# Kernel optimization log

Measured on AMD Instinct MI355X. Metric: run time of the kernel, lower is better.

Reference implementation:

```python
import jax, jax.numpy as jnp
import numpy as np

EPS = 1e-5

def layer_norm(x, g, b):
    m = jnp.mean(x, axis=-1, keepdims=True)
    v = jnp.mean((x - m) ** 2, axis=-1, keepdims=True)
    return (x - m) * jax.lax.rsqrt(v + EPS) * g + b

def conv1d(x, w, b, pad):
    # x: [B, C_in, L], w: [C_out, C_in, K]
    y = jax.lax.conv_general_dilated(x, w, (1,), [(pad, pad)],
                                     dimension_numbers=('NCH', 'OIH', 'NCH'))
    return y + b[None, :, None]

def setup_inputs() -> dict:
    key = jax.random.key(0)
    B, L, D, H, W, HID = 8, 1024, 512, 8, 3, 64
    ks = jax.random.split(key, 32)
    s = 0.02
    inp = {}
    inp['x'] = jax.random.normal(ks[0], (B, L, D), jnp.float32)
    # WaveDetector convs
    inp['conv1_w'] = jax.random.normal(ks[1], (HID, D, 5), jnp.float32) * s
    inp['conv1_b'] = jnp.zeros((HID,), jnp.float32)
    inp['conv2_w'] = jax.random.normal(ks[2], (HID, HID, 3), jnp.float32) * s
    inp['conv2_b'] = jnp.zeros((HID,), jnp.float32)
    inp['conv3_w'] = jax.random.normal(ks[3], (W, HID, 3), jnp.float32) * s
    inp['conv3_b'] = jnp.zeros((W,), jnp.float32)
    # wave type embedding
    inp['wave_emb'] = jax.random.normal(ks[4], (W, D), jnp.float32) * s
    # attention projections (stored as [in, out])
    inp['wq_w'] = jax.random.normal(ks[5], (D, D), jnp.float32) * s
    inp['wq_b'] = jnp.zeros((D,), jnp.float32)
    inp['wk_w'] = jax.random.normal(ks[6], (D, D), jnp.float32) * s
    inp['wk_b'] = jnp.zeros((D,), jnp.float32)
    inp['wv_w'] = jax.random.normal(ks[7], (D, D), jnp.float32) * s
    inp['wv_b'] = jnp.zeros((D,), jnp.float32)
    # gate MLP: D -> D//4 -> H
    inp['g1_w'] = jax.random.normal(ks[8], (D, D // 4), jnp.float32) * s
    inp['g1_b'] = jnp.zeros((D // 4,), jnp.float32)
    inp['g2_w'] = jax.random.normal(ks[9], (D // 4, H), jnp.float32) * s
    inp['g2_b'] = jnp.zeros((H,), jnp.float32)
    # layer norms
    for i, nm in enumerate(['ln_attn', 'norm1', 'ln_conv', 'norm2', 'norm3']):
        inp[nm + '_g'] = jnp.ones((D,), jnp.float32) + jax.random.normal(ks[10 + i], (D,), jnp.float32) * 0.01
        inp[nm + '_b'] = jax.random.normal(ks[15 + i], (D,), jnp.float32) * 0.01
    # subgraph conv: one Linear per wave + wave weights
    inp['wc_w'] = jax.random.normal(ks[20], (W, D, D), jnp.float32) * s
    inp['wc_b'] = jnp.zeros((W, D), jnp.float32)
    inp['wave_weights'] = jnp.ones((W,), jnp.float32) / W
    # FFN
    inp['f1_w'] = jax.random.normal(ks[21], (D, 4 * D), jnp.float32) * s
    inp['f1_b'] = jnp.zeros((4 * D,), jnp.float32)
    inp['f2_w'] = jax.random.normal(ks[22], (4 * D, D), jnp.float32) * s
    inp['f2_b'] = jnp.zeros((D,), jnp.float32)
    return inp

def reference(x, conv1_w, conv1_b, conv2_w, conv2_b, conv3_w, conv3_b, wave_emb,
              wq_w, wq_b, wk_w, wk_b, wv_w, wv_b, g1_w, g1_b, g2_w, g2_b,
              ln_attn_g, ln_attn_b, norm1_g, norm1_b, wc_w, wc_b, wave_weights,
              ln_conv_g, ln_conv_b, norm2_g, norm2_b, f1_w, f1_b, f2_w, f2_b,
              norm3_g, norm3_b):
    B, L, D = x.shape
    H = g2_w.shape[1]
    hd = D // H
    # --- WaveDetector ---
    xt = jnp.swapaxes(x, 1, 2)                       # [B, D, L]
    h = jax.nn.relu(conv1d(xt, conv1_w, conv1_b, 2))
    h = jax.nn.relu(conv1d(h, conv2_w, conv2_b, 1))
    wp = conv1d(h, conv3_w, conv3_b, 1)              # [B, W, L]
    wave_mask = jax.nn.softmax(jnp.swapaxes(wp, 1, 2), axis=-1)  # [B, L, W]
    # --- WaveTypeEncoding ---
    labels = jnp.argmax(wave_mask, axis=-1)          # [B, L] int
    x = x + wave_emb[labels]
    # --- subgraph adjacency (base_adj = ones) ---
    wave_sim = jnp.einsum('blw,bmw->blm', wave_mask, wave_mask)  # [B, L, L]
    subgraph_adj = wave_sim
    # --- DynamicWaveAttention ---
    residual = x
    Q = (x @ wq_w + wq_b).reshape(B, L, H, hd)
    K = (x @ wk_w + wk_b).reshape(B, L, H, hd)
    V = (x @ wv_w + wv_b).reshape(B, L, H, hd)
    scores = jnp.einsum('bqhd,bkhd->bhqk', Q, K) / (hd ** 0.5)
    gates = jax.nn.sigmoid(jax.nn.relu(x @ g1_w + g1_b) @ g2_w + g2_b)  # [B, L, H]
    gates = jnp.transpose(gates, (0, 2, 1))[:, :, None, :]              # [B, H, 1, L]
    scores = scores * gates + scores * wave_sim[:, None]
    scores = scores + subgraph_adj[:, None]
    attn = jax.nn.softmax(scores, axis=-1)
    attn_out = jnp.einsum('bhqk,bkhd->bqhd', attn, V).reshape(B, L, D)
    attn_out = layer_norm(attn_out + residual, ln_attn_g, ln_attn_b)
    x = layer_norm(x + attn_out, norm1_g, norm1_b)
    # --- ECGSubGraphConv (adj_matrices=None path) ---
    feats = jnp.einsum('bld,wdo->blwo', x, wc_w) + wc_b          # [B, L, W, D]
    conv_out = jnp.einsum('blwo,blw,w->blo', feats, wave_mask, wave_weights)
    conv_out = layer_norm(jax.nn.relu(conv_out), ln_conv_g, ln_conv_b)
    x = layer_norm(x + conv_out, norm2_g, norm2_b)
    # --- FFN ---
    ffn = jax.nn.relu(x @ f1_w + f1_b) @ f2_w + f2_b
    x = layer_norm(x + ffn, norm3_g, norm3_b)
    return (x, wave_mask, subgraph_adj)
```

## Files before the change

kernel.cpp:

```cpp
#include <hip/hip_runtime.h>

typedef unsigned short u16;
typedef unsigned int u32;
typedef __attribute__((ext_vector_type(8))) short bf16x8;
typedef __attribute__((ext_vector_type(4))) float f32x4;
typedef __attribute__((ext_vector_type(4))) u32 u32x4;

#define DEVI static __device__ __forceinline__

constexpr size_t OFF_WTQKV = 0;
constexpr size_t OFF_G1T   = 1572864;
constexpr size_t OFF_G2T   = OFF_G1T + 131072;
constexpr size_t OFF_WCT   = OFF_G2T + 2048;
constexpr size_t OFF_F1T   = OFF_WCT + 1572864;
constexpr size_t OFF_F2T   = OFF_F1T + 2097152;
constexpr size_t OFF_W1R   = OFF_F2T + 2097152;
constexpr size_t OFF_W2R   = OFF_W1R + 655360;
constexpr size_t OFF_H1    = OFF_W2R + 49152;
constexpr size_t OFF_GMID  = OFF_H1;
constexpr size_t OFF_GATES = OFF_H1 + 2097152;
constexpr size_t OFF_X1    = OFF_GATES + 262144;
constexpr size_t OFF_X3    = OFF_X1;
constexpr size_t OFF_X1B   = OFF_X1 + 16777216;
constexpr size_t OFF_FMID  = OFF_X1B;
constexpr size_t OFF_Q     = OFF_X1B + 8388608;
constexpr size_t OFF_H1P   = OFF_Q;
constexpr size_t OFF_K     = OFF_Q + 8388608;
constexpr size_t OFF_XH    = OFF_K;
constexpr size_t OFF_VT    = OFF_K + 8388608;
constexpr size_t OFF_XL    = OFF_VT + 32768;
constexpr size_t OFF_AO    = OFF_VT + 8388608;
constexpr size_t OFF_CONV  = OFF_AO;
constexpr size_t OFF_FP0   = OFF_AO;
constexpr size_t OFF_X2    = OFF_AO + 16777216;
constexpr size_t OFF_FP1   = OFF_X2;
constexpr size_t OFF_X2B   = OFF_X2 + 16777216;
constexpr size_t OFF_X3B   = OFF_X2B;

DEVI u16 f2bf(float f) {
  u32 u = __builtin_bit_cast(u32, f);
  u32 r = (u + 0x7FFFu + ((u >> 16) & 1u)) >> 16;
  return (u16)r;
}
DEVI float bf2f(u16 h) { u32 u = ((u32)h) << 16; return __builtin_bit_cast(float, u); }

DEVI void load8(const float* __restrict__ p, float o[8]) {
  const float4* q = (const float4*)p;
  float4 a = q[0], b = q[1];
  o[0]=a.x; o[1]=a.y; o[2]=a.z; o[3]=a.w; o[4]=b.x; o[5]=b.y; o[6]=b.z; o[7]=b.w;
}
DEVI void store8(float* __restrict__ p, const float o[8]) {
  float4 a; a.x=o[0]; a.y=o[1]; a.z=o[2]; a.w=o[3];
  float4 b; b.x=o[4]; b.y=o[5]; b.z=o[6]; b.w=o[7];
  float4* q = (float4*)p; q[0]=a; q[1]=b;
}
DEVI void store8bf(u16* __restrict__ p, const float o[8]) {
  u32 w[4];
#pragma unroll
  for (int i=0;i<4;i++) w[i] = (u32)f2bf(o[2*i]) | ((u32)f2bf(o[2*i+1]) << 16);
  u32x4 v; v.x=w[0]; v.y=w[1]; v.z=w[2]; v.w=w[3];
  *(u32x4*)p = v;
}

DEVI void gl_lds16(const u16* g, u16* l) {
  __builtin_amdgcn_global_load_lds((const __attribute__((address_space(1))) u32*)g,
                                   (__attribute__((address_space(3))) u32*)l, 16, 0, 0);
}

#define PIPE_WAIT(N)  asm volatile("s_waitcnt vmcnt(%0)" :: "n"(N) : "memory")
#define PIPE_WAIT0()  asm volatile("s_waitcnt vmcnt(0)" ::: "memory")
#define PIPE_BAR()    do { __builtin_amdgcn_s_barrier(); asm volatile("" ::: "memory"); } while (0)
#define PIPE_BAR_LGKM() do { asm volatile("s_waitcnt lgkmcnt(0)" ::: "memory"); \
                             __builtin_amdgcn_s_barrier(); asm volatile("" ::: "memory"); } while (0)

__global__ __launch_bounds__(64) void prep_kernel(
    const float* s0, const float* s1, const float* s2, const float* s3, const float* s4,
    const float* s5, const float* s6, const float* s7, const float* s8, const float* s9,
    char* ws) {
  const int jsrc[11] = {0,1,2,3,4, 5,5,5, 6,7, 9};
  const int jK[11]   = {512,512,512,512,128, 512,512,512, 512,2048, 64};
  const int jN[11]   = {512,512,512,128,8,   512,512,512, 2048,512, 192};
  const int jSo[11]  = {0,0,0,0,0, 0,262144,524288, 0,0, 0};
  const long long jDo[11] = {
    (long long)OFF_WTQKV, (long long)(OFF_WTQKV+524288), (long long)(OFF_WTQKV+1048576),
    (long long)OFF_G1T, (long long)OFF_G2T,
    (long long)OFF_WCT, (long long)(OFF_WCT+524288), (long long)(OFF_WCT+1048576),
    (long long)OFF_F1T, (long long)OFF_F2T, (long long)OFF_W2R};
  const int jF[11]   = {0,0,0,0,0,0,0,0,0,0,1};

  int blk = blockIdx.x;
  int j = 0, t = 0;
  for (int i = 0; i < 11; i++) {
    int cnt = ((jK[i] + 63) >> 6) * ((jN[i] + 63) >> 6);
    if (blk < cnt) { j = i; t = blk; break; }
    blk -= cnt;
  }
  int K = jK[j], N = jN[j];
  int ktiles = (K + 63) >> 6;
  int k0 = (t % ktiles) << 6, n0 = (t / ktiles) << 6;
  const float* SS[10] = {s0,s1,s2,s3,s4,s5,s6,s7,s8,s9};
  const float* src = SS[jsrc[j]] + jSo[j];
  __shared__ float tile[64][65];
  int tt = threadIdx.x;
  for (int i = 0; i < 64; i++) {
    float v = 0.f;
    if (k0 + i < K && n0 + tt < N) v = src[(size_t)(k0 + i) * N + n0 + tt];
    tile[i][tt] = v;
  }
  __syncthreads();
  if (jF[j]) {
    float* dst = (float*)(ws + jDo[j]);
    for (int i = 0; i < 64; i++)
      if (n0 + i < N && k0 + tt < K) dst[(size_t)(n0 + i) * K + k0 + tt] = tile[tt][i];
  } else {
    u16* dst = (u16*)(ws + jDo[j]);
    for (int i = 0; i < 64; i++)
      if (n0 + i < N && k0 + tt < K) dst[(size_t)(n0 + i) * K + k0 + tt] = f2bf(tile[tt][i]);
  }
}

__global__ __launch_bounds__(256) void wprep_kernel(const float* __restrict__ w1,
                                                    u16* __restrict__ wh, u16* __restrict__ wl) {
  int c = blockIdx.x;
  for (int kk = threadIdx.x; kk < 2560; kk += 256) {
    int k = kk >> 9, d = kk & 511;
    float v = w1[(size_t)c * 2560 + d * 5 + k];
    u16 h = f2bf(v);
    wh[(size_t)c * 2560 + kk] = h;
    wl[(size_t)c * 2560 + kk] = f2bf(v - bf2f(h));
  }
}

__global__ __launch_bounds__(256) void xsplit_kernel(const float* __restrict__ x,
                                                     u16* __restrict__ xh, u16* __restrict__ xl) {
  int idx = blockIdx.x * 256 + threadIdx.x;
  if (idx >= 8 * 1028 * 64) return;
  int r = idx >> 6;
  int col = (idx & 63) * 8;
  int b = r / 1028, rr = r % 1028;
  size_t dof = ((size_t)r) * 512 + col;
  if (rr < 2 || rr >= 1026) {
    u32x4 z; z.x = 0; z.y = 0; z.z = 0; z.w = 0;
    *(u32x4*)&xh[dof] = z;
    *(u32x4*)&xl[dof] = z;
    return;
  }
  const float* src = x + (((size_t)b << 10) + rr - 2) * 512 + col;
  float v[8];
  load8(src, v);
  u32 wh_[4], wl_[4];
#pragma unroll
  for (int i = 0; i < 4; i++) {
    u16 h0 = f2bf(v[2 * i]),     l0 = f2bf(v[2 * i]     - bf2f(f2bf(v[2 * i])));
    u16 h1 = f2bf(v[2 * i + 1]), l1 = f2bf(v[2 * i + 1] - bf2f(f2bf(v[2 * i + 1])));
    wh_[i] = (u32)h0 | ((u32)h1 << 16);
    wl_[i] = (u32)l0 | ((u32)l1 << 16);
  }
  u32x4 H; H.x=wh_[0]; H.y=wh_[1]; H.z=wh_[2]; H.w=wh_[3];
  u32x4 L; L.x=wl_[0]; L.y=wl_[1]; L.z=wl_[2]; L.w=wl_[3];
  *(u32x4*)&xh[dof] = H;
  *(u32x4*)&xl[dof] = L;
}

__global__ __launch_bounds__(256, 6) void conv1g_kernel(
    const u16* __restrict__ xh, const u16* __restrict__ xl,
    const u16* __restrict__ wh, const u16* __restrict__ wl,
    float* __restrict__ h1p) {
  __shared__ alignas(16) u16 a_s[2][64 * 32];
  __shared__ alignas(16) u16 b_s[2][64 * 32];
  const int tid = threadIdx.x, lane = tid & 63, wid = tid >> 6;
  const int m0 = blockIdx.x * 64;
  const int z = blockIdx.z;
  const int wr = wid >> 1, wc = wid & 1;
  const int mb = wr * 32, nb = wc * 32;
  const int lrow = lane & 15, lk = (lane >> 4) * 8;
  const int lr4 = lane >> 2, lc8 = (lane & 3) * 8;
  const int bb = m0 >> 10, lblk = m0 & 1023;
  const size_t xrow0 = (size_t)bb * 1028;

  auto stage = [&](int buf, int kk) {
    int p = (kk >= 5120) ? 2 : (kk >= 2560) ? 1 : 0;
    int kpp = kk - p * 2560;
    int ktap = kpp >> 9, d0 = kpp & 511;
    const u16* xa = (p == 1) ? xl : xh;
    const u16* wb = (p == 2) ? wl : wh;
    gl_lds16(&xa[(xrow0 + lblk + wid * 16 + lr4 + ktap) * 512 + d0 + lc8],
             &a_s[buf][wid * 512]);
    gl_lds16(&wb[(size_t)(wid * 16 + lr4) * 2560 + kpp + lc8],
             &b_s[buf][wid * 512]);
  };

  f32x4 acc[2][2];
#pragma unroll
  for (int m = 0; m < 2; m++)
#pragma unroll
    for (int n = 0; n < 2; n++) { acc[m][n].x=0.f; acc[m][n].y=0.f; acc[m][n].z=0.f; acc[m][n].w=0.f; }

  const int kz0 = z * 1920, kz1 = kz0 + 1920;
  stage(0, kz0);
  int cur = 0;
  for (int kk = kz0; kk < kz1; kk += 32) {
    if (kk + 32 < kz1) {
      stage(cur ^ 1, kk + 32);
      PIPE_WAIT(2);
    } else {
      PIPE_WAIT0();
    }
    PIPE_BAR();
    bf16x8 af[2], bfr[2];
#pragma unroll
    for (int m = 0; m < 2; m++) af[m]  = *(const bf16x8*)&a_s[cur][(mb + m * 16 + lrow) * 32 + lk];
#pragma unroll
    for (int n = 0; n < 2; n++) bfr[n] = *(const bf16x8*)&b_s[cur][(nb + n * 16 + lrow) * 32 + lk];
#pragma unroll
    for (int m = 0; m < 2; m++)
#pragma unroll
      for (int n = 0; n < 2; n++)
        acc[m][n] = __builtin_amdgcn_mfma_f32_16x16x32_bf16(af[m], bfr[n], acc[m][n], 0, 0, 0);
    PIPE_BAR_LGKM();
    cur ^= 1;
  }
  const int r4 = (lane >> 4) * 4;
#pragma unroll
  for (int m = 0; m < 2; m++) {
#pragma unroll
    for (int n = 0; n < 2; n++) {
      const int col = nb + n * 16 + lrow;
#pragma unroll
      for (int j = 0; j < 4; j++) {
        const int row = m0 + mb + m * 16 + r4 + j;
        h1p[(size_t)z * 524288 + (size_t)row * 64 + col] = acc[m][n][j];
      }
    }
  }
}

__global__ __launch_bounds__(256) void conv23_kernel(
    const float* __restrict__ h1p, const float* __restrict__ b1,
    const float* __restrict__ w2r, const float* __restrict__ b2,
    const float* __restrict__ w3, const float* __restrict__ b3,
    const float* __restrict__ x, const float* __restrict__ emb,
    float* __restrict__ wmOut, float* __restrict__ x1, u16* __restrict__ x1b) {
  int seg = blockIdx.x;
  int batch = seg >> 5, l0 = (seg & 31) << 5;
  int tid = threadIdx.x, lane = tid & 63, wave = tid >> 6;
  __shared__ float hs[36][64];
  __shared__ float h2s[34][65];
  __shared__ float w3s[576];
  __shared__ int labS[32];
  for (int i = tid; i < 36 * 64; i += 256) {
    int r = i >> 6, cc = i & 63;
    int lp = l0 - 2 + r;
    float v = 0.f;
    if (lp >= 0 && lp < 1024) {
      size_t base = ((size_t)batch * 1024 + lp) * 64 + cc;
      float s = b1[cc];
#pragma unroll
      for (int q = 0; q < 4; q++) s += h1p[base + (size_t)q * 524288];
      v = fmaxf(s, 0.f);
    }
    hs[r][cc] = v;
  }
  for (int i = tid; i < 576; i += 256) w3s[i] = w3[i];
  __syncthreads();
  {
    int c = lane;
    int r0 = wave * 9;
    float a2[9];
#pragma unroll
    for (int i = 0; i < 9; i++) a2[i] = b2[c];
    for (int dd = 0; dd < 64; dd++) {
      float xv[11];
#pragma unroll
      for (int i = 0; i < 11; i++) xv[i] = (r0 + i < 36) ? hs[r0 + i][dd] : 0.f;
#pragma unroll
      for (int k = 0; k < 3; k++) {
        float wv = w2r[(size_t)(dd * 3 + k) * 64 + c];
#pragma unroll
        for (int i = 0; i < 9; i++) a2[i] += xv[i + k] * wv;
      }
    }
#pragma unroll
    for (int i = 0; i < 9; i++) {
      int hr = r0 + i;
      if (hr < 34) h2s[hr][c] = fmaxf(a2[i], 0.f);
    }
  }
  __syncthreads();
  if (tid < 32) {
    float wp[3];
#pragma unroll
    for (int jw = 0; jw < 3; jw++) {
      float a = b3[jw];
      for (int k = 0; k < 3; k++)
        for (int cc = 0; cc < 64; cc++)
          a += h2s[tid + k][cc] * w3s[(jw * 64 + cc) * 3 + k];
      wp[jw] = a;
    }
    float mx = fmaxf(wp[0], fmaxf(wp[1], wp[2]));
    float e0 = __expf(wp[0] - mx), e1 = __expf(wp[1] - mx), e2 = __expf(wp[2] - mx);
    float inv = 1.f / (e0 + e1 + e2);
    size_t mo = ((size_t)batch * 1024 + l0 + tid) * 3;
    wmOut[mo] = e0 * inv; wmOut[mo + 1] = e1 * inv; wmOut[mo + 2] = e2 * inv;
    int lb = 0; float bv = wp[0];
    if (wp[1] > bv) { bv = wp[1]; lb = 1; }
    if (wp[2] > bv) { lb = 2; }
    labS[tid] = lb;
  }
  __syncthreads();
  for (int i = tid; i < 32 * 512; i += 256) {
    int r = i >> 9, cc = i & 511;
    size_t gi = ((size_t)batch * 1024 + l0 + r) * 512 + cc;
    float v = x[gi] + emb[labS[r] * 512 + cc];
    x1[gi] = v;
    x1b[gi] = f2bf(v);
  }
}

__global__ __launch_bounds__(256) void wavesim_kernel(const float* __restrict__ wm,
                                                      float* __restrict__ adj) {
  int b = blockIdx.x >> 7;
  int r0 = (blockIdx.x & 127) << 3;
  __shared__ float ms[1024][3];
  int tid = threadIdx.x;
  for (int i = tid; i < 3072; i += 256) ms[i / 3][i % 3] = wm[(size_t)b * 3072 + i];
  __syncthreads();
  for (int r = 0; r < 8; r++) {
    float a0 = ms[r0 + r][0], a1 = ms[r0 + r][1], a2 = ms[r0 + r][2];
    for (int m = tid; m < 1024; m += 256)
      adj[((size_t)b * 1024 + r0 + r) * 1024 + m] = a0 * ms[m][0] + a1 * ms[m][1] + a2 * ms[m][2];
  }
}

struct GemmArgs {
  const u16* A; const u16* Bt;
  int lda; int ldb; int K;
  const float* bias;
  u16* obf; int ldo;
  float* of32; int ldo32;
  u16* Qo; u16* Ko; u16* Vto;
  const float* bq; const float* bk; const float* bv;
};

template<int BM, int BN, int FM, int FN, int EPI>
__global__ __launch_bounds__(256, 3) void gemm_k(GemmArgs p) {
  __shared__ alignas(16) u16 a_s[2][BM * 32];
  __shared__ alignas(16) u16 b_s[2][BN * 32];
  const int tid = threadIdx.x;
  const int lane = tid & 63, wid = tid >> 6;
  const int m0 = blockIdx.x * BM, n0 = blockIdx.y * BN;
  const int koff = (EPI == 6) ? blockIdx.z * p.K : 0;
  const int wr = wid >> 1, wc = wid & 1;
  const int mb = wr * (FM * 16), nb = wc * (FN * 16);
  const int lrow = lane & 15, lk = (lane >> 4) * 8;
  constexpr int CPW_A = BM / 64;
  constexpr int CPW_B = BN / 64;
  constexpr int NL = CPW_A + CPW_B;
  const int lr4 = lane >> 2, lc8 = (lane & 3) * 8;

  auto stage = [&](int buf, int k0) {
#pragma unroll
    for (int j = 0; j < CPW_A; j++) {
      int chunk = wid * CPW_A + j;
      gl_lds16(&p.A[(size_t)(m0 + chunk * 16 + lr4) * p.lda + koff + k0 + lc8],
               &a_s[buf][chunk * 512]);
    }
#pragma unroll
    for (int j = 0; j < CPW_B; j++) {
      int chunk = wid * CPW_B + j;
      gl_lds16(&p.Bt[(size_t)(n0 + chunk * 16 + lr4) * p.ldb + koff + k0 + lc8],
               &b_s[buf][chunk * 512]);
    }
  };

  f32x4 acc[FM][FN];
#pragma unroll
  for (int m = 0; m < FM; m++)
#pragma unroll
    for (int n = 0; n < FN; n++) { acc[m][n].x=0.f; acc[m][n].y=0.f; acc[m][n].z=0.f; acc[m][n].w=0.f; }

  stage(0, 0);
  int cur = 0;
  for (int k0 = 0; k0 < p.K; k0 += 32) {
    if (k0 + 32 < p.K) {
      stage(cur ^ 1, k0 + 32);
      PIPE_WAIT(NL);
    } else {
      PIPE_WAIT0();
    }
    PIPE_BAR();
    bf16x8 af[FM], bfr[FN];
#pragma unroll
    for (int m = 0; m < FM; m++) af[m] = *(const bf16x8*)&a_s[cur][(mb + m * 16 + lrow) * 32 + lk];
#pragma unroll
    for (int n = 0; n < FN; n++) bfr[n] = *(const bf16x8*)&b_s[cur][(nb + n * 16 + lrow) * 32 + lk];
#pragma unroll
    for (int m = 0; m < FM; m++)
#pragma unroll
      for (int n = 0; n < FN; n++)
        acc[m][n] = __builtin_amdgcn_mfma_f32_16x16x32_bf16(af[m], bfr[n], acc[m][n], 0, 0, 0);
    PIPE_BAR_LGKM();
    cur ^= 1;
  }
  const int r4 = (lane >> 4) * 4;
#pragma unroll
  for (int m = 0; m < FM; m++) {
#pragma unroll
    for (int n = 0; n < FN; n++) {
      const int col = n0 + nb + n * 16 + lrow;
#pragma unroll
      for (int j = 0; j < 4; j++) {
        const int row = m0 + mb + m * 16 + r4 + j;
        float v = acc[m][n][j];
        if constexpr (EPI == 1) {
          v += p.bias[col];
          v = fmaxf(v, 0.f);
          p.obf[(size_t)row * p.ldo + col] = f2bf(v);
        } else if constexpr (EPI == 2) {
          v += p.bias[col];
          p.of32[(size_t)row * p.ldo32 + col] = v;
        } else if constexpr (EPI == 3) {
          if (col < 512) {
            v += p.bq[col];
            p.Qo[(size_t)row * 512 + col] = f2bf(v);
          } else if (col < 1024) {
            int cc = col - 512;
            v += p.bk[cc];
            p.Ko[(size_t)row * 512 + cc] = f2bf(v);
          } else if (col < 1536) {
            int cc = col - 1024;
            v += p.bv[cc];
            int hh = cc >> 6, dd = cc & 63;
            int bb2 = row >> 10, ll = row & 1023;
            p.Vto[((((size_t)bb2 * 8 + hh) * 64 + dd) << 10) + ll] = f2bf(v);
          } else {
            int cc = col - 1536;
            v += p.bias[cc];
            v = fmaxf(v, 0.f);
            p.obf[(size_t)row * 128 + cc] = f2bf(v);
          }
        } else if constexpr (EPI == 6) {
          if (blockIdx.z == 0) v += p.bias[col];
          p.of32[(size_t)blockIdx.z * p.ldo32 + (size_t)row * 512 + col] = v;
        }
      }
    }
  }
}

__global__ __launch_bounds__(256) void wcg_kernel(
    const u16* __restrict__ A, const u16* __restrict__ Wct,
    const float* __restrict__ wcb, const float* __restrict__ wmask,
    const float* __restrict__ wwts, float* __restrict__ out) {
  __shared__ alignas(16) u16 a_s[2][128 * 32];
  __shared__ alignas(16) u16 b_s[2][3 * 64 * 32];
  const int tid = threadIdx.x, lane = tid & 63, wid = tid >> 6;
  const int m0 = blockIdx.x * 128, n0 = blockIdx.y * 64;
  const int wr = wid >> 1, wc = wid & 1;
  const int mb = wr * 64, nb = wc * 32;
  const int lrow = lane & 15, lk = (lane >> 4) * 8;
  const int lr4 = lane >> 2, lc8 = (lane & 3) * 8;

  auto stage = [&](int buf, int k0) {
#pragma unroll
    for (int t = 0; t < 2; t++) {
      int ch = wid * 2 + t;
      gl_lds16(&A[(size_t)(m0 + ch * 16 + lr4) * 512 + k0 + lc8], &a_s[buf][ch * 512]);
    }
#pragma unroll
    for (int t = 0; t < 3; t++) {
      int ch = wid * 3 + t;
      int wI = ch >> 2, sub = ch & 3;
      gl_lds16(&Wct[(size_t)wI * 262144 + (size_t)(n0 + sub * 16 + lr4) * 512 + k0 + lc8],
               &b_s[buf][ch * 512]);
    }
  };

  f32x4 acc[4][2][3];
#pragma unroll
  for (int m = 0; m < 4; m++)
#pragma unroll
    for (int n = 0; n < 2; n++)
#pragma unroll
      for (int w = 0; w < 3; w++) { acc[m][n][w].x=0.f; acc[m][n][w].y=0.f; acc[m][n][w].z=0.f; acc[m][n][w].w=0.f; }

  stage(0, 0);
  int cur = 0;
  for (int k0 = 0; k0 < 512; k0 += 32) {
    if (k0 + 32 < 512) {
      stage(cur ^ 1, k0 + 32);
      PIPE_WAIT(5);
    } else {
      PIPE_WAIT0();
    }
    PIPE_BAR();
    bf16x8 af[4], bfr[3][2];
#pragma unroll
    for (int m = 0; m < 4; m++) af[m] = *(const bf16x8*)&a_s[cur][(mb + m * 16 + lrow) * 32 + lk];
#pragma unroll
    for (int w = 0; w < 3; w++)
#pragma unroll
      for (int n = 0; n < 2; n++)
        bfr[w][n] = *(const bf16x8*)&b_s[cur][(w * 64 + nb + n * 16 + lrow) * 32 + lk];
#pragma unroll
    for (int m = 0; m < 4; m++)
#pragma unroll
      for (int n = 0; n < 2; n++)
#pragma unroll
        for (int w = 0; w < 3; w++)
          acc[m][n][w] = __builtin_amdgcn_mfma_f32_16x16x32_bf16(af[m], bfr[w][n], acc[m][n][w], 0, 0, 0);
    PIPE_BAR_LGKM();
    cur ^= 1;
  }
  const float w0 = wwts[0], w1 = wwts[1], w2 = wwts[2];
  const int r4 = (lane >> 4) * 4;
#pragma unroll
  for (int m = 0; m < 4; m++) {
#pragma unroll
    for (int j = 0; j < 4; j++) {
      const int row = m0 + mb + m * 16 + r4 + j;
      float c0 = wmask[(size_t)row * 3 + 0] * w0;
      float c1 = wmask[(size_t)row * 3 + 1] * w1;
      float c2 = wmask[(size_t)row * 3 + 2] * w2;
#pragma unroll
      for (int n = 0; n < 2; n++) {
        const int col = n0 + nb + n * 16 + lrow;
        float v = c0 * (acc[m][n][0][j] + wcb[col])
                + c1 * (acc[m][n][1][j] + wcb[512 + col])
                + c2 * (acc[m][n][2][j] + wcb[1024 + col]);
        out[(size_t)row * 512 + col] = v;
      }
    }
  }
}

__global__ __launch_bounds__(256) void gates2_kernel(const u16* __restrict__ gmid,
    const u16* __restrict__ g2t, const float* __restrict__ g2b, float* __restrict__ gates) {
  int r0 = blockIdx.x * 64;
  __shared__ u16 ms[64][136];
  __shared__ u16 gs[8][136];
  __shared__ float gb[8];
  int tid = threadIdx.x;
  for (int i = tid; i < 1024; i += 256) {
    int r = i >> 4, ch = (i & 15) * 8;
    *(bf16x8*)&ms[r][ch] = *(const bf16x8*)&gmid[(size_t)(r0 + r) * 128 + ch];
  }
  if (tid < 128) {
    int r = tid >> 4, ch = (tid & 15) * 8;
    *(bf16x8*)&gs[r][ch] = *(const bf16x8*)&g2t[(size_t)r * 128 + ch];
  }
  if (tid < 8) gb[tid] = g2b[tid];
  __syncthreads();
  for (int o = tid; o < 512; o += 256) {
    int r = o >> 3, hh = o & 7;
    float a = gb[hh];
    for (int k = 0; k < 128; k++) a += bf2f(ms[r][k]) * bf2f(gs[hh][k]);
    gates[(size_t)(r0 + r) * 8 + hh] = 1.f / (1.f + __expf(-a));
  }
}

__global__ __launch_bounds__(256, 4) void attn_kernel(
    const u16* __restrict__ Qb, const u16* __restrict__ Kb, const u16* __restrict__ Vt,
    const float* __restrict__ gates, const float* __restrict__ wm, float* __restrict__ ao) {
  const int g = blockIdx.x & 63, qt = blockIdx.x >> 6;
  const int b = g >> 3, h = g & 7, q0 = qt << 6;
  const int tid = threadIdx.x, lane = tid & 63, w = tid >> 6;
  __shared__ alignas(16) u16 k_s[64 * 64];
  __shared__ alignas(16) u16 v_s[64 * 64];
  __shared__ u16 p_s[4][16][72];
  __shared__ float gat[64];
  __shared__ float wmk[64][4];
  const int lrow = lane & 15, lq = lane >> 4, lk = lq * 8;
  const int qrb = q0 + w * 16;
  const int sr_ = lane >> 3, sc_ = lane & 7;
  bf16x8 qf[2];
#pragma unroll
  for (int ks = 0; ks < 2; ks++)
    qf[ks] = *(const bf16x8*)&Qb[((size_t)(b * 1024 + qrb + lrow)) * 512 + h * 64 + ks * 32 + lk];
  float wq_[4][3];
#pragma unroll
  for (int j = 0; j < 4; j++) {
    int qr = qrb + lq * 4 + j;
#pragma unroll
    for (int t = 0; t < 3; t++) wq_[j][t] = wm[((size_t)b * 1024 + qr) * 3 + t];
  }
  float lsum[4];
  f32x4 oacc[4];
#pragma unroll
  for (int j = 0; j < 4; j++) lsum[j] = 0.f;
#pragma unroll
  for (int n = 0; n < 4; n++) { oacc[n].x=0.f; oacc[n].y=0.f; oacc[n].z=0.f; oacc[n].w=0.f; }

  const u16* Kbase = Kb + ((size_t)b * 1024) * 512 + h * 64;
  const u16* Vbase = Vt + ((size_t)(b * 8 + h)) * 64 * 1024;

  for (int kt = 0; kt < 16; kt++) {
    int k0 = kt * 64;
    __syncthreads();
#pragma unroll
    for (int t = 0; t < 2; t++) {
      int ch = (w << 1) | t;
      int r = (ch << 3) | sr_;
      int srcc = ((sc_ ^ (r & 7)) << 3);
      gl_lds16(&Kbase[(size_t)(k0 + r) * 512 + srcc], &k_s[ch << 9]);
      gl_lds16(&Vbase[(size_t)r * 1024 + k0 + srcc], &v_s[ch << 9]);
    }
    if (tid < 64) {
      gat[tid] = gates[((size_t)b * 1024 + k0 + tid) * 8 + h];
#pragma unroll
      for (int t = 0; t < 3; t++) wmk[tid][t] = wm[((size_t)b * 1024 + k0 + tid) * 3 + t];
    }
    __syncthreads();
    f32x4 s[4];
#pragma unroll
    for (int n = 0; n < 4; n++) { s[n].x=0.f; s[n].y=0.f; s[n].z=0.f; s[n].w=0.f; }
#pragma unroll
    for (int ks = 0; ks < 2; ks++) {
      bf16x8 kf[4];
#pragma unroll
      for (int n = 0; n < 4; n++) {
        int kr = n * 16 + lrow;
        kf[n] = *(const bf16x8*)&k_s[kr * 64 + ((((ks << 2) | lq) ^ (kr & 7)) << 3)];
      }
#pragma unroll
      for (int n = 0; n < 4; n++)
        s[n] = __builtin_amdgcn_mfma_f32_16x16x32_bf16(qf[ks], kf[n], s[n], 0, 0, 0);
    }
    float pv[4][4];
#pragma unroll
    for (int n = 0; n < 4; n++) {
      int cl = n * 16 + lrow;
      float gg = gat[cl];
      float w0 = wmk[cl][0], w1 = wmk[cl][1], w2 = wmk[cl][2];
#pragma unroll
      for (int j = 0; j < 4; j++) {
        float wsv = wq_[j][0] * w0 + wq_[j][1] * w1 + wq_[j][2] * w2;
        float sv = s[n][j] * 0.125f;
        float e = __expf(sv * (gg + wsv) + wsv);
        pv[n][j] = e;
        lsum[j] += e;
      }
    }
#pragma unroll
    for (int n = 0; n < 4; n++)
#pragma unroll
      for (int j = 0; j < 4; j++)
        p_s[w][lq * 4 + j][n * 16 + lrow] = f2bf(pv[n][j]);
#pragma unroll
    for (int ks = 0; ks < 2; ks++) {
      bf16x8 pa, vb[4];
      pa = *(const bf16x8*)&p_s[w][lrow][ks * 32 + lk];
#pragma unroll
      for (int n = 0; n < 4; n++) {
        int vr = n * 16 + lrow;
        vb[n] = *(const bf16x8*)&v_s[vr * 64 + ((((ks << 2) | lq) ^ (vr & 7)) << 3)];
      }
#pragma unroll
      for (int n = 0; n < 4; n++)
        oacc[n] = __builtin_amdgcn_mfma_f32_16x16x32_bf16(pa, vb[n], oacc[n], 0, 0, 0);
    }
  }
  float rinv[4];
#pragma unroll
  for (int j = 0; j < 4; j++) {
    float s = lsum[j];
#pragma unroll
    for (int d = 1; d < 16; d <<= 1) s += __shfl_xor(s, d);
    rinv[j] = 1.f / s;
  }
#pragma unroll
  for (int n = 0; n < 4; n++) {
    int col = h * 64 + n * 16 + lrow;
#pragma unroll
    for (int j = 0; j < 4; j++) {
      int row = b * 1024 + qrb + lq * 4 + j;
      ao[(size_t)row * 512 + col] = oacc[n][j] * rinv[j];
    }
  }
}

DEVI void ln512(const float u[8], const float* __restrict__ g, const float* __restrict__ b,
                int lane, float out[8]) {
  float s = 0.f;
#pragma unroll
  for (int i = 0; i < 8; i++) s += u[i];
#pragma unroll
  for (int m = 1; m < 64; m <<= 1) s += __shfl_xor(s, m);
  float mean = s * (1.f / 512.f);
  float d[8], q = 0.f;
#pragma unroll
  for (int i = 0; i < 8; i++) { d[i] = u[i] - mean; q += d[i] * d[i]; }
#pragma unroll
  for (int m = 1; m < 64; m <<= 1) q += __shfl_xor(q, m);
  float inv = rsqrtf(q * (1.f / 512.f) + 1e-5f);
  int base = lane * 8;
#pragma unroll
  for (int i = 0; i < 8; i++) out[i] = d[i] * inv * g[base + i] + b[base + i];
}

__global__ __launch_bounds__(256) void ln1_kernel(
    const float* __restrict__ ao, const float* __restrict__ x1,
    const float* __restrict__ ga, const float* __restrict__ gb,
    const float* __restrict__ n1g, const float* __restrict__ n1b,
    float* __restrict__ x2, u16* __restrict__ x2b) {
  int row = blockIdx.x * 4 + (threadIdx.x >> 6);
  int lane = threadIdx.x & 63;
  size_t base = (size_t)row * 512 + lane * 8;
  float av[8], xv[8], u[8], t[8];
  load8(ao + base, av);
  load8(x1 + base, xv);
#pragma unroll
  for (int i = 0; i < 8; i++) u[i] = av[i] + xv[i];
  ln512(u, ga, gb, lane, t);
#pragma unroll
  for (int i = 0; i < 8; i++) u[i] = xv[i] + t[i];
  ln512(u, n1g, n1b, lane, t);
  store8(x2 + base, t);
  store8bf(x2b + base, t);
}

__global__ __launch_bounds__(256) void ln2_kernel(
    const float* __restrict__ co, const float* __restrict__ x2,
    const float* __restrict__ gc, const float* __restrict__ bc,
    const float* __restrict__ n2g, const float* __restrict__ n2b,
    float* __restrict__ x3, u16* __restrict__ x3b) {
  int row = blockIdx.x * 4 + (threadIdx.x >> 6);
  int lane = threadIdx.x & 63;
  size_t base = (size_t)row * 512 + lane * 8;
  float av[8], xv[8], u[8], t[8];
  load8(co + base, av);
#pragma unroll
  for (int i = 0; i < 8; i++) u[i] = fmaxf(av[i], 0.f);
  ln512(u, gc, bc, lane, t);
  load8(x2 + base, xv);
#pragma unroll
  for (int i = 0; i < 8; i++) u[i] = xv[i] + t[i];
  ln512(u, n2g, n2b, lane, t);
  store8(x3 + base, t);
  store8bf(x3b + base, t);
}

__global__ __launch_bounds__(256) void ln3_kernel(
    const float* __restrict__ x3, const float* __restrict__ p0, const float* __restrict__ p1,
    const float* __restrict__ n3g, const float* __restrict__ n3b,
    float* __restrict__ out0) {
  int row = blockIdx.x * 4 + (threadIdx.x >> 6);
  int lane = threadIdx.x & 63;
  size_t base = (size_t)row * 512 + lane * 8;
  float a0[8], a1[8], xv[8], u[8], t[8];
  load8(x3 + base, xv);
  load8(p0 + base, a0);
  load8(p1 + base, a1);
#pragma unroll
  for (int i = 0; i < 8; i++) u[i] = xv[i] + a0[i] + a1[i];
  ln512(u, n3g, n3b, lane, t);
  store8(out0 + base, t);
}

extern "C" void kernel_launch(void* const* d_in, const int* in_sizes, int n_in,
                              void* d_out, int out_size, void* d_ws, size_t ws_size,
                              hipStream_t stream) {
  const float* x    = (const float*)d_in[0];
  const float* w1   = (const float*)d_in[1];
  const float* c1b  = (const float*)d_in[2];
  const float* w2   = (const float*)d_in[3];
  const float* c2b  = (const float*)d_in[4];
  const float* w3   = (const float*)d_in[5];
  const float* c3b  = (const float*)d_in[6];
  const float* emb  = (const float*)d_in[7];
  const float* wqw  = (const float*)d_in[8];
  const float* wqb  = (const float*)d_in[9];
  const float* wkw  = (const float*)d_in[10];
  const float* wkb  = (const float*)d_in[11];
  const float* wvw  = (const float*)d_in[12];
  const float* wvb  = (const float*)d_in[13];
  const float* g1w  = (const float*)d_in[14];
  const float* g1b  = (const float*)d_in[15];
  const float* g2w  = (const float*)d_in[16];
  const float* g2b  = (const float*)d_in[17];
  const float* lag  = (const float*)d_in[18];
  const float* lab  = (const float*)d_in[19];
  const float* n1g  = (const float*)d_in[20];
  const float* n1b  = (const float*)d_in[21];
  const float* lcg  = (const float*)d_in[22];
  const float* lcb  = (const float*)d_in[23];
  const float* n2g  = (const float*)d_in[24];
  const float* n2b  = (const float*)d_in[25];
  const float* n3g  = (const float*)d_in[26];
  const float* n3b  = (const float*)d_in[27];
  const float* wcw  = (const float*)d_in[28];
  const float* wcb  = (const float*)d_in[29];
  const float* wwts = (const float*)d_in[30];
  const float* f1w  = (const float*)d_in[31];
  const float* f1b  = (const float*)d_in[32];
  const float* f2w  = (const float*)d_in[33];
  const float* f2b  = (const float*)d_in[34];

  char* ws = (char*)d_ws;
  float* out0 = (float*)d_out;
  float* out1 = out0 + 4194304;
  float* out2 = out1 + 24576;

  float* w2r_p  = (float*)(ws + OFF_W2R);
  u16*   wh_p   = (u16*)(ws + OFF_W1R);
  u16*   wl_p   = (u16*)(ws + OFF_W1R + 327680);
  u16*   xh_p   = (u16*)(ws + OFF_XH);
  u16*   xl_p   = (u16*)(ws + OFF_XL);
  float* h1p_p  = (float*)(ws + OFF_H1P);
  float* x1_p   = (float*)(ws + OFF_X1);
  u16*   x1b_p  = (u16*)(ws + OFF_X1B);
  u16*   wtqkv  = (u16*)(ws + OFF_WTQKV);
  u16*   g2t_p  = (u16*)(ws + OFF_G2T);
  u16*   wct_p  = (u16*)(ws + OFF_WCT);
  u16*   f1t_p  = (u16*)(ws + OFF_F1T);
  u16*   f2t_p  = (u16*)(ws + OFF_F2T);
  u16*   q_p    = (u16*)(ws + OFF_Q);
  u16*   k_p    = (u16*)(ws + OFF_K);
  u16*   vt_p   = (u16*)(ws + OFF_VT);
  u16*   gmid_p = (u16*)(ws + OFF_GMID);
  float* gates_p= (float*)(ws + OFF_GATES);
  float* ao_p   = (float*)(ws + OFF_AO);
  float* x2_p   = (float*)(ws + OFF_X2);
  u16*   x2b_p  = (u16*)(ws + OFF_X2B);
  float* conv_p = (float*)(ws + OFF_CONV);
  float* x3_p   = (float*)(ws + OFF_X3);
  u16*   x3b_p  = (u16*)(ws + OFF_X3B);
  u16*   fmid_p = (u16*)(ws + OFF_FMID);
  float* fp0_p  = (float*)(ws + OFF_FP0);
  float* fp1_p  = (float*)(ws + OFF_FP1);

  prep_kernel<<<917, 64, 0, stream>>>(wqw, wkw, wvw, g1w, g2w, wcw, f1w, f2w, w1, w2, ws);
  wprep_kernel<<<64, 256, 0, stream>>>(w1, wh_p, wl_p);
  xsplit_kernel<<<2056, 256, 0, stream>>>(x, xh_p, xl_p);
  conv1g_kernel<<<dim3(128, 1, 4), 256, 0, stream>>>(xh_p, xl_p, wh_p, wl_p, h1p_p);
  conv23_kernel<<<256, 256, 0, stream>>>(h1p_p, c1b, w2r_p, c2b, w3, c3b, x, emb, out1, x1_p, x1b_p);
  wavesim_kernel<<<1024, 256, 0, stream>>>(out1, out2);
  {
    GemmArgs a{}; a.A = x1b_p; a.lda = 512; a.Bt = wtqkv; a.ldb = 512; a.K = 512;
    a.Qo = q_p; a.Ko = k_p; a.Vto = vt_p; a.bq = wqb; a.bk = wkb; a.bv = wvb;
    a.bias = g1b; a.obf = gmid_p; a.ldo = 128;
    gemm_k<128,128,4,4,3><<<dim3(64,13), 256, 0, stream>>>(a);
  }
  gates2_kernel<<<128, 256, 0, stream>>>(gmid_p, g2t_p, g2b, gates_p);
  attn_kernel<<<1024, 256, 0, stream>>>(q_p, k_p, vt_p, gates_p, out1, ao_p);
  ln1_kernel<<<2048, 256, 0, stream>>>(ao_p, x1_p, lag, lab, n1g, n1b, x2_p, x2b_p);
  wcg_kernel<<<dim3(64, 8), 256, 0, stream>>>(x2b_p, wct_p, wcb, out1, wwts, conv_p);
  ln2_kernel<<<2048, 256, 0, stream>>>(conv_p, x2_p, lcg, lcb, n2g, n2b, x3_p, x3b_p);
  {
    GemmArgs a{}; a.A = x3b_p; a.lda = 512; a.Bt = f1t_p; a.ldb = 512; a.K = 512;
    a.bias = f1b; a.obf = fmid_p; a.ldo = 2048;
    gemm_k<128,128,4,4,1><<<dim3(64,16), 256, 0, stream>>>(a);
  }
  {
    GemmArgs a{}; a.A = fmid_p; a.lda = 2048; a.Bt = f2t_p; a.ldb = 2048; a.K = 1024;
    a.bias = f2b; a.of32 = fp0_p; a.ldo32 = 4194304;
    gemm_k<128,128,4,4,6><<<dim3(64,4,2), 256, 0, stream>>>(a);
  }
  ln3_kernel<<<2048, 256, 0, stream>>>(x3_p, fp0_p, fp1_p, n3g, n3b, out0);

  (void)in_sizes; (void)n_in; (void)out_size; (void)ws_size;
}
```

Baseline: 323.0 us.

## Halve conv23 segment length, parallelize conv3 reduction, vectorize embedding add

Splits each sequence into 16-row segments instead of 32, doubling the grid of conv23 to 512 blocks so more CUs are busy. The conv3/softmax stage, previously done by 32 threads serially over 192 products, now uses all 256 threads with 16-lane shuffle reductions. The embedding-add/bf16 store loop uses float4 loads and packed stores. The cost is more halo recomputation per block (20 rows for 16 outputs vs 36 for 32).

```diff
diff --git a/kernel.cpp b/kernel.cpp
--- a/kernel.cpp
+++ b/kernel.cpp
@@ -242,13 +242,13 @@
     const float* __restrict__ x, const float* __restrict__ emb,
     float* __restrict__ wmOut, float* __restrict__ x1, u16* __restrict__ x1b) {
   int seg = blockIdx.x;
-  int batch = seg >> 5, l0 = (seg & 31) << 5;
+  int batch = seg >> 6, l0 = (seg & 63) << 4;
   int tid = threadIdx.x, lane = tid & 63, wave = tid >> 6;
-  __shared__ float hs[36][64];
-  __shared__ float h2s[34][65];
+  __shared__ float hs[20][64];
+  __shared__ float h2s[18][65];
   __shared__ float w3s[576];
-  __shared__ int labS[32];
-  for (int i = tid; i < 36 * 64; i += 256) {
+  __shared__ int labS[16];
+  for (int i = tid; i < 20 * 64; i += 256) {
     int r = i >> 6, cc = i & 63;
     int lp = l0 - 2 + r;
     float v = 0.f;
@@ -265,55 +265,73 @@
   __syncthreads();
   {
     int c = lane;
-    int r0 = wave * 9;
-    float a2[9];
-#pragma unroll
-    for (int i = 0; i < 9; i++) a2[i] = b2[c];
+    int r0 = wave * 5;
+    float a2[5];
+#pragma unroll
+    for (int i = 0; i < 5; i++) a2[i] = b2[c];
     for (int dd = 0; dd < 64; dd++) {
-      float xv[11];
-#pragma unroll
-      for (int i = 0; i < 11; i++) xv[i] = (r0 + i < 36) ? hs[r0 + i][dd] : 0.f;
+      float xv[7];
+#pragma unroll
+      for (int i = 0; i < 7; i++) xv[i] = (r0 + i < 20) ? hs[r0 + i][dd] : 0.f;
 #pragma unroll
       for (int k = 0; k < 3; k++) {
         float wv = w2r[(size_t)(dd * 3 + k) * 64 + c];
 #pragma unroll
-        for (int i = 0; i < 9; i++) a2[i] += xv[i + k] * wv;
+        for (int i = 0; i < 5; i++) a2[i] += xv[i + k] * wv;
       }
     }
 #pragma unroll
-    for (int i = 0; i < 9; i++) {
+    for (int i = 0; i < 5; i++) {
       int hr = r0 + i;
-      if (hr < 34) h2s[hr][c] = fmaxf(a2[i], 0.f);
+      if (hr < 18) h2s[hr][c] = fmaxf(a2[i], 0.f);
     }
   }
   __syncthreads();
-  if (tid < 32) {
+  {
+    int li = tid >> 4, g = tid & 15;
+    int c0 = g * 4;
     float wp[3];
 #pragma unroll
     for (int jw = 0; jw < 3; jw++) {
-      float a = b3[jw];
+      float a = 0.f;
+#pragma unroll
       for (int k = 0; k < 3; k++)
-        for (int cc = 0; cc < 64; cc++)
-          a += h2s[tid + k][cc] * w3s[(jw * 64 + cc) * 3 + k];
+#pragma unroll
+        for (int c = 0; c < 4; c++)
+          a += h2s[li + k][c0 + c] * w3s[(jw * 64 + c0 + c) * 3 + k];
       wp[jw] = a;
     }
-    float mx = fmaxf(wp[0], fmaxf(wp[1], wp[2]));
-    float e0 = __expf(wp[0] - mx), e1 = __expf(wp[1] - mx), e2 = __expf(wp[2] - mx);
-    float inv = 1.f / (e0 + e1 + e2);
-    size_t mo = ((size_t)batch * 1024 + l0 + tid) * 3;
-    wmOut[mo] = e0 * inv; wmOut[mo + 1] = e1 * inv; wmOut[mo + 2] = e2 * inv;
-    int lb = 0; float bv = wp[0];
-    if (wp[1] > bv) { bv = wp[1]; lb = 1; }
-    if (wp[2] > bv) { lb = 2; }
-    labS[tid] = lb;
+#pragma unroll
+    for (int d = 1; d < 16; d <<= 1) {
+#pragma unroll
+      for (int jw = 0; jw < 3; jw++) wp[jw] += __shfl_xor(wp[jw], d);
+    }
+    if (g == 0) {
+      float wp0 = wp[0] + b3[0], wp1 = wp[1] + b3[1], wp2 = wp[2] + b3[2];
+      float mx = fmaxf(wp0, fmaxf(wp1, wp2));
+      float e0 = __expf(wp0 - mx), e1 = __expf(wp1 - mx), e2 = __expf(wp2 - mx);
+      float inv = 1.f / (e0 + e1 + e2);
+      size_t mo = ((size_t)batch * 1024 + l0 + li) * 3;
+      wmOut[mo] = e0 * inv; wmOut[mo + 1] = e1 * inv; wmOut[mo + 2] = e2 * inv;
+      int lb = 0; float bv = wp0;
+      if (wp1 > bv) { bv = wp1; lb = 1; }
+      if (wp2 > bv) { lb = 2; }
+      labS[li] = lb;
+    }
   }
   __syncthreads();
-  for (int i = tid; i < 32 * 512; i += 256) {
-    int r = i >> 9, cc = i & 511;
-    size_t gi = ((size_t)batch * 1024 + l0 + r) * 512 + cc;
-    float v = x[gi] + emb[labS[r] * 512 + cc];
-    x1[gi] = v;
-    x1b[gi] = f2bf(v);
+  for (int i = tid; i < 16 * 128; i += 256) {
+    int r = i >> 7, cq = (i & 127) << 2;
+    size_t gi = ((size_t)batch * 1024 + l0 + r) * 512 + cq;
+    float4 xv = *(const float4*)&x[gi];
+    const float* ep = &emb[(size_t)labS[r] * 512 + cq];
+    float4 ev = *(const float4*)ep;
+    float4 v; v.x = xv.x + ev.x; v.y = xv.y + ev.y; v.z = xv.z + ev.z; v.w = xv.w + ev.w;
+    *(float4*)&x1[gi] = v;
+    u32 lo = (u32)f2bf(v.x) | ((u32)f2bf(v.y) << 16);
+    u32 hi = (u32)f2bf(v.z) | ((u32)f2bf(v.w) << 16);
+    *(u32*)&x1b[gi] = lo;
+    *(u32*)&x1b[gi + 2] = hi;
   }
 }
 
@@ -833,7 +851,7 @@
   wprep_kernel<<<64, 256, 0, stream>>>(w1, wh_p, wl_p);
   xsplit_kernel<<<2056, 256, 0, stream>>>(x, xh_p, xl_p);
   conv1g_kernel<<<dim3(128, 1, 4), 256, 0, stream>>>(xh_p, xl_p, wh_p, wl_p, h1p_p);
-  conv23_kernel<<<256, 256, 0, stream>>>(h1p_p, c1b, w2r_p, c2b, w3, c3b, x, emb, out1, x1_p, x1b_p);
+  conv23_kernel<<<512, 256, 0, stream>>>(h1p_p, c1b, w2r_p, c2b, w3, c3b, x, emb, out1, x1_p, x1b_p);
   wavesim_kernel<<<1024, 256, 0, stream>>>(out1, out2);
   {
     GemmArgs a{}; a.A = x1b_p; a.lda = 512; a.Bt = wtqkv; a.ldb = 512; a.K = 512;
```

New measurement: 308.5 us. 1.05x faster.
